# Kernel tuning notes

Measured on AMD Instinct MI355X. Metric: run time of the kernel, lower is better.

Reference implementation:

```python
import jax, jax.numpy as jnp
import numpy as np

LN_EPS = 1e-5
ATT_EPS = 1e-6

def layer_norm(x, scale, bias):
    mu = jnp.mean(x, axis=-1, keepdims=True)
    var = jnp.mean(jnp.square(x - mu), axis=-1, keepdims=True)
    return (x - mu) * jax.lax.rsqrt(var + LN_EPS) * scale + bias

def setup_inputs() -> dict:
    key = jax.random.key(0)
    ks = jax.random.split(key, 8)
    N, C, H = 16384, 1024, 8
    s = 0.02
    return {
        "x": jax.random.normal(ks[0], (N, C), dtype=jnp.float32),
        "Wq": jax.random.normal(ks[1], (C, C), dtype=jnp.float32) * s,
        "Wkv": jax.random.normal(ks[2], (C, 2 * C), dtype=jnp.float32) * s,
        "ln1_scale": jnp.ones((C,), dtype=jnp.float32),
        "ln1_bias": jnp.zeros((C,), dtype=jnp.float32),
        "W1": jax.random.normal(ks[3], (C, C), dtype=jnp.float32) * s,
        "b1": jnp.zeros((C,), dtype=jnp.float32),
        "W2": jax.random.normal(ks[4], (C, C), dtype=jnp.float32) * s,
        "b2": jnp.zeros((C,), dtype=jnp.float32),
        "ln2_scale": jnp.ones((C,), dtype=jnp.float32),
        "ln2_bias": jnp.zeros((C,), dtype=jnp.float32),
    }

def reference(x, Wq, Wkv, ln1_scale, ln1_bias, W1, b1, W2, b2, ln2_scale, ln2_bias):
    H = 8
    N, C = x.shape
    d = C // H
    # QKV projections; torch .view(-1, d, heads) splits last dim as (d, H)
    q = (x @ Wq).reshape(N, d, H)
    kv = x @ Wkv  # [N, 2C]
    k = kv[:, :C].reshape(N, d, H)
    v = kv[:, C:].reshape(N, d, H)
    # Kernelized linear attention per head (phi = elu + 1), global segment (bi=None)
    phi_q = jax.nn.elu(q) + 1.0
    phi_k = jax.nn.elu(k) + 1.0
    kv_sum = jnp.einsum('ndh,neh->deh', phi_k, v)      # [d, d, H]
    z = jnp.sum(phi_k, axis=0)                          # [d, H]
    num = jnp.einsum('ndh,deh->neh', phi_q, kv_sum)     # [N, d, H]
    den = jnp.einsum('ndh,dh->nh', phi_q, z)            # [N, H]
    t = (num / (den[:, None, :] + ATT_EPS)).reshape(N, C)
    # AddNorm (beta=False, dropout=0): ln(t + x)
    y = layer_norm(t + x, ln1_scale, ln1_bias)
    # FFN: Linear -> GELU (exact) -> Linear
    h = jax.nn.gelu(y @ W1 + b1, approximate=False)
    f = h @ W2 + b2
    return layer_norm(f + y, ln2_scale, ln2_bias)
```

## Files before the change

kernel.cpp:

```cpp
#include <hip/hip_runtime.h>
#include <hip/hip_bf16.h>
#include <cstdint>
#include <cstddef>

typedef __bf16 bf16_t;
typedef bf16_t bf16x4 __attribute__((ext_vector_type(4)));
typedef bf16_t bf16x8 __attribute__((ext_vector_type(8)));
typedef float f32x4 __attribute__((ext_vector_type(4)));

static constexpr int NROWS = 16384;
static constexpr int CDIM  = 1024;

__device__ __forceinline__ int p6(int k) {
  return (k & 32) | ((k & 12) << 1) | ((k & 16) >> 2) | (k & 3);
}
__device__ __forceinline__ int p6i(int s) {
  return (s & 32) | ((s & 4) << 2) | ((s & 24) >> 1) | (s & 3);
}
__device__ __forceinline__ int permc(int c) {
  return (c & ~63) | p6(c & 63);
}


__device__ __forceinline__ void gload16(const bf16_t* g, bf16_t* l) {
  __builtin_amdgcn_global_load_lds((const __attribute__((address_space(1))) void*)g,
                                   (__attribute__((address_space(3))) void*)l, 16, 0, 0);
}

__device__ __forceinline__ bf16x8 ldsf128(const bf16_t* lds, int row, int ldbytes, int kbyte) {
  const char* p = (const char*)lds + row * ldbytes + (kbyte ^ ((row & 7) << 4));
  return *(const bf16x8*)p;
}

__device__ __forceinline__ float phi_fn(float v) {
  return v > 0.f ? v + 1.f : expf(v);
}
__device__ __forceinline__ float gelu_fn(float v) {
  return 0.5f * v * (1.f + erff(v * 0.70710678118654752f));
}


__global__ void cast_x_kernel(const float* __restrict__ x, bf16_t* __restrict__ xb, long nchunks) {
  long i = (long)blockIdx.x * blockDim.x + threadIdx.x;
  long stride = (long)gridDim.x * blockDim.x;
  for (long c = i; c < nchunks; c += stride) {
    long row = c >> 7;
    int p0 = (int)(c & 127) << 3;
    int group = p0 & ~63;
    int ccl = (p0 >> 3) & 7;
    int klo = ((ccl & 4) << 3) | ((ccl & 3) << 2);
    const float* src = x + row * 1024 + group + klo;
    float4 a = *(const float4*)src;
    float4 b = *(const float4*)(src + 16);
    bf16x8 o;
    o[0] = (bf16_t)a.x; o[1] = (bf16_t)a.y; o[2] = (bf16_t)a.z; o[3] = (bf16_t)a.w;
    o[4] = (bf16_t)b.x; o[5] = (bf16_t)b.y; o[6] = (bf16_t)b.z; o[7] = (bf16_t)b.w;
    *(bf16x8*)(xb + row * 1024 + p0) = o;
  }
}

__global__ void prep_w_kernel(const float* __restrict__ Wq, const float* __restrict__ Wkv,
                              const float* __restrict__ W1, const float* __restrict__ W2,
                              bf16_t* __restrict__ wqkv_bt, bf16_t* __restrict__ w1bt,
                              bf16_t* __restrict__ w2bt) {
  __shared__ float tile[64][65];
  int mode = blockIdx.z;
  const float* src; int ld; bf16_t* dst; int permute;
  if (mode == 0)      { src = Wq;          ld = 1024; dst = wqkv_bt;                       permute = 1; }
  else if (mode == 1) { src = Wkv;         ld = 2048; dst = wqkv_bt + (size_t)1024 * 1024; permute = 1; }
  else if (mode == 2) { src = Wkv + 1024;  ld = 2048; dst = wqkv_bt + (size_t)2048 * 1024; permute = 1; }
  else if (mode == 3) { src = W1;          ld = 1024; dst = w1bt;                          permute = 0; }
  else                { src = W2;          ld = 1024; dst = w2bt;                          permute = 0; }
  int r0 = blockIdx.x * 64, c0 = blockIdx.y * 64;
  int tid = threadIdx.x;
#pragma unroll
  for (int i = 0; i < 16; i++) {
    int idx = i * 256 + tid; int rr = idx >> 6, cc = idx & 63;
    tile[rr][cc] = src[(size_t)(r0 + rr) * ld + c0 + cc];
  }
  __syncthreads();
#pragma unroll
  for (int i = 0; i < 16; i++) {
    int idx = i * 256 + tid; int cc = idx >> 6, rr = idx & 63;
    int c = c0 + cc;
    int a = permute ? (((c & 7) << 7) | (c >> 3)) : c;
    dst[(size_t)a * 1024 + r0 + p6(rr)] = (bf16_t)tile[rr][cc];
  }
}


template<int MODE>
__global__ __launch_bounds__(256, 4)
void gemm_bt_kernel(const bf16_t* __restrict__ A, const bf16_t* __restrict__ Bt,
                    const float* __restrict__ bias,
                    bf16_t* __restrict__ o0, bf16_t* __restrict__ o1, bf16_t* __restrict__ o2,
                    int M, int N, int K)
{
  __shared__ bf16_t As[128 * 64];
  __shared__ bf16_t Bs[128 * 64];
  const int tid  = threadIdx.x;
  const int lane = tid & 63;
  const int wave = tid >> 6;
  const int wr = (wave >> 1) * 64, wc = (wave & 1) * 64;
  const int l15 = lane & 15, g = lane >> 4;
  const int row0 = blockIdx.x * 128, col0 = blockIdx.y * 128;
  const int cb = wave * 256;
  f32x4 acc[4][4] = {};

  for (int kt = 0; kt < K; kt += 64) {
    __syncthreads();
#pragma unroll
    for (int it = 0; it < 4; ++it) {
      int ch = cb + it * 64 + lane;
      int r = ch >> 3;
      int csrc = (ch & 7) ^ (r & 7);
      gload16(A  + (size_t)(row0 + r) * K + kt + csrc * 8, As + (size_t)(cb + it * 64) * 8);
      gload16(Bt + (size_t)(col0 + r) * K + kt + csrc * 8, Bs + (size_t)(cb + it * 64) * 8);
    }
    __syncthreads();
#pragma unroll
    for (int ks = 0; ks < 2; ++ks) {
      bf16x8 af[4], bfr[4];
#pragma unroll
      for (int i = 0; i < 4; i++) af[i]  = ldsf128(As, wr + i * 16 + l15, 128, ks * 64 + 16 * g);
#pragma unroll
      for (int i = 0; i < 4; i++) bfr[i] = ldsf128(Bs, wc + i * 16 + l15, 128, ks * 64 + 16 * g);
#pragma unroll
      for (int i = 0; i < 4; i++)
#pragma unroll
        for (int j = 0; j < 4; j++)
          acc[i][j] = __builtin_amdgcn_mfma_f32_16x16x32_bf16(af[i], bfr[j], acc[i][j], 0, 0, 0);
    }
  }

#pragma unroll
  for (int i = 0; i < 4; i++) {
    int rbase = row0 + wr + i * 16 + g * 4;
#pragma unroll
    for (int j = 0; j < 4; j++) {
      int col = col0 + wc + j * 16 + l15;
      f32x4 v = acc[i][j];
      if constexpr (MODE == 0) {
        int seg = col >> 10;
        int cl  = permc(col & 1023);
        bf16_t* dst = (seg == 0) ? o0 : (seg == 1 ? o1 : o2);
#pragma unroll
        for (int rr = 0; rr < 4; rr++) {
          float val = v[rr];
          if (seg != 2) val = phi_fn(val);
          dst[(size_t)(rbase + rr) * 1024 + cl] = (bf16_t)val;
        }
      } else if constexpr (MODE == 1) {
        float bv = bias[col];
        int cs = permc(col);
#pragma unroll
        for (int rr = 0; rr < 4; rr++)
          o0[(size_t)(rbase + rr) * 1024 + cs] = (bf16_t)gelu_fn(v[rr] + bv);
      } else {
        float bv = bias[col];
#pragma unroll
        for (int rr = 0; rr < 4; rr++)
          o0[(size_t)(rbase + rr) * 1024 + col] = (bf16_t)(v[rr] + bv);
      }
    }
  }
}


__global__ __launch_bounds__(256, 4)
void kvsum_kernel(const bf16_t* __restrict__ phik, const bf16_t* __restrict__ vb,
                  float* __restrict__ P, float* __restrict__ Zp)
{
  __shared__ bf16_t kls[64 * 128];
  __shared__ bf16_t vls[64 * 128];
  const int h = blockIdx.y;
  const int c = blockIdx.x;
  const int n0 = c * 256;
  const int tid = threadIdx.x;
  const int lane = tid & 63, wave = tid >> 6;
  const int cb = wave * 256;
  const int ek0 = (tid >> 4) * 8, ev0 = (tid & 15) * 8;
  float acc[8][8] = {};
  float zacc[8] = {};

  for (int nt = 0; nt < 4; ++nt) {
    __syncthreads();
#pragma unroll
    for (int it = 0; it < 4; ++it) {
      int ch = cb + it * 64 + lane;
      int r = ch >> 4, c16 = ch & 15;
      const size_t gsrc = (size_t)(n0 + nt * 64 + r) * 1024 + h * 128 + c16 * 8;
      gload16(phik + gsrc, kls + (size_t)(cb + it * 64) * 8);
      gload16(vb   + gsrc, vls + (size_t)(cb + it * 64) * 8);
    }
    __syncthreads();
#pragma unroll 2
    for (int n = 0; n < 64; n++) {
      bf16x8 a8 = *(const bf16x8*)(kls + n * 128 + ek0);
      bf16x8 b8 = *(const bf16x8*)(vls + n * 128 + ev0);
      float a[8], b[8];
#pragma unroll
      for (int i = 0; i < 8; i++) { a[i] = (float)a8[i]; b[i] = (float)b8[i]; }
      if ((tid & 15) == 0) {
#pragma unroll
        for (int i = 0; i < 8; i++) zacc[i] += a[i];
      }
#pragma unroll
      for (int i = 0; i < 8; i++)
#pragma unroll
        for (int j = 0; j < 8; j++) acc[i][j] += a[i] * b[j];
    }
  }
  float* pb = P + ((size_t)h * 64 + c) * 16384;
#pragma unroll
  for (int i = 0; i < 8; i++) {
    *(float4*)(pb + (ek0 + i) * 128 + ev0)     = *(float4*)&acc[i][0];
    *(float4*)(pb + (ek0 + i) * 128 + ev0 + 4) = *(float4*)&acc[i][4];
  }
  if ((tid & 15) == 0) {
    float* zb = Zp + ((size_t)h * 64 + c) * 128;
#pragma unroll
    for (int i = 0; i < 8; i++) zb[ek0 + i] = zacc[i];
  }
}

__global__ void reduce_kvsum_kernel(const float* __restrict__ P, const float* __restrict__ Zp,
                                    bf16_t* __restrict__ Mbt, float* __restrict__ z)
{
  int i = blockIdx.x * 256 + threadIdx.x;
  int h = i >> 14, ds = (i >> 7) & 127, fs = i & 127;
  const float* p = P + (size_t)h * 64 * 16384 + (size_t)ds * 128 + fs;
  float s = 0.f;
#pragma unroll 8
  for (int c = 0; c < 64; ++c) s += p[(size_t)c * 16384];
  int fl = (fs & 64) | p6i(fs & 63);
  Mbt[(size_t)h * 16384 + fl * 128 + ds] = (bf16_t)s;
  if (i < 1024) {
    int hh = i >> 7, dd = i & 127;
    const float* q = Zp + (size_t)hh * 64 * 128 + dd;
    float sz = 0.f;
#pragma unroll 8
    for (int c = 0; c < 64; ++c) sz += q[c * 128];
    z[i] = sz;
  }
}


__global__ __launch_bounds__(256, 2)
void attn_t_kernel(const bf16_t* __restrict__ phiq, const bf16_t* __restrict__ Mbt,
                   const float* __restrict__ z, bf16_t* __restrict__ tout)
{
  __shared__ bf16_t As[64 * 128];
  __shared__ bf16_t Bs[128 * 128];
  __shared__ float  zs[128];
  __shared__ float  dens[64];
  int h = blockIdx.y, row0 = blockIdx.x * 64;
  int tid = threadIdx.x, lane = tid & 63, wave = tid >> 6;
  int wr = (wave >> 1) * 32, wc = (wave & 1) * 64;
  int l15 = lane & 15, g = lane >> 4;

#pragma unroll
  for (int it = 0; it < 4; ++it) {
    int ch = it * 256 + tid;
    int r = ch >> 4, c8 = ch & 15;
    int cs = c8 ^ (r & 7);
    *(bf16x8*)(As + r * 128 + cs * 8) = *(const bf16x8*)(phiq + (size_t)(row0 + r) * 1024 + h * 128 + c8 * 8);
  }
#pragma unroll
  for (int it = 0; it < 8; ++it) {
    int ch = it * 256 + tid;
    int r = ch >> 4, c8 = ch & 15;
    int cs = c8 ^ (r & 7);
    *(bf16x8*)(Bs + r * 128 + cs * 8) = *(const bf16x8*)(Mbt + (size_t)h * 16384 + ch * 8);
  }
  if (tid < 128) zs[tid] = z[h * 128 + tid];
  __syncthreads();

  f32x4 acc[2][4] = {};
#pragma unroll
  for (int ks = 0; ks < 4; ++ks) {
    bf16x8 af[2], bfr[4];
#pragma unroll
    for (int i = 0; i < 2; i++) af[i]  = ldsf128(As, wr + i * 16 + l15, 256, ks * 64 + 16 * g);
#pragma unroll
    for (int j = 0; j < 4; j++) bfr[j] = ldsf128(Bs, wc + j * 16 + l15, 256, ks * 64 + 16 * g);
#pragma unroll
    for (int i = 0; i < 2; i++)
#pragma unroll
      for (int j = 0; j < 4; j++)
        acc[i][j] = __builtin_amdgcn_mfma_f32_16x16x32_bf16(af[i], bfr[j], acc[i][j], 0, 0, 0);
  }

  if (tid < 64) {
    float s = 0.f;
    const char* p = (const char*)As + tid * 256;
    int sw = (tid & 7) << 4;
    for (int d0 = 0; d0 < 128; ++d0) {
      int d = (d0 + tid) & 127;
      bf16_t kv = *(const bf16_t*)(p + ((2 * d) ^ sw));
      s += (float)kv * zs[d];
    }
    dens[tid] = s;
  }
  __syncthreads();

#pragma unroll
  for (int i = 0; i < 2; i++) {
    int lr = wr + i * 16 + g * 4;
#pragma unroll
    for (int j = 0; j < 4; j++) {
      int col = h * 128 + wc + j * 16 + l15;
      f32x4 v = acc[i][j];
#pragma unroll
      for (int rr = 0; rr < 4; rr++) {
        float den = dens[lr + rr] + 1e-6f;
        tout[(size_t)(row0 + lr + rr) * 1024 + col] = (bf16_t)(v[rr] / den);
      }
    }
  }
}


__global__ __launch_bounds__(256, 2)
void ln1_kernel(const bf16_t* __restrict__ t, const float* __restrict__ x,
                const float* __restrict__ gma, const float* __restrict__ bta,
                bf16_t* __restrict__ y)
{
  __shared__ float s[1024];
  __shared__ float rsum[4], rsq[4];
  int n = blockIdx.x, tid = threadIdx.x;
#pragma unroll
  for (int k = 0; k < 4; k++) {
    int p = k * 256 + tid;
    float tv = (float)t[(size_t)n * 1024 + p];
    int c = ((p & 127) << 3) | (p >> 7);
    s[c] = tv;
  }
  __syncthreads();
  float sum = 0.f, sq = 0.f, sv[4];
#pragma unroll
  for (int k = 0; k < 4; k++) {
    int c = k * 256 + tid;
    float v = s[c] + x[(size_t)n * 1024 + c];
    sv[k] = v; sum += v; sq += v * v;
  }
#pragma unroll
  for (int o = 32; o > 0; o >>= 1) { sum += __shfl_down(sum, o); sq += __shfl_down(sq, o); }
  if ((tid & 63) == 0) { rsum[tid >> 6] = sum; rsq[tid >> 6] = sq; }
  __syncthreads();
  sum = rsum[0] + rsum[1] + rsum[2] + rsum[3];
  sq  = rsq[0] + rsq[1] + rsq[2] + rsq[3];
  float mu = sum * (1.f / 1024.f);
  float var = sq * (1.f / 1024.f) - mu * mu;
  float rs = rsqrtf(var + 1e-5f);
#pragma unroll
  for (int k = 0; k < 4; k++) {
    int c = k * 256 + tid;
    y[(size_t)n * 1024 + permc(c)] = (bf16_t)((sv[k] - mu) * rs * gma[c] + bta[c]);
  }
}

__global__ __launch_bounds__(256, 2)
void ln2_kernel(const bf16_t* __restrict__ f, const bf16_t* __restrict__ y,
                const float* __restrict__ gma, const float* __restrict__ bta,
                float* __restrict__ out)
{
  __shared__ float rsum[4], rsq[4];
  int n = blockIdx.x, tid = threadIdx.x;
  float sum = 0.f, sq = 0.f, sv[4];
#pragma unroll
  for (int k = 0; k < 4; k++) {
    int c = k * 256 + tid;
    float v = (float)f[(size_t)n * 1024 + c] + (float)y[(size_t)n * 1024 + permc(c)];
    sv[k] = v; sum += v; sq += v * v;
  }
#pragma unroll
  for (int o = 32; o > 0; o >>= 1) { sum += __shfl_down(sum, o); sq += __shfl_down(sq, o); }
  if ((tid & 63) == 0) { rsum[tid >> 6] = sum; rsq[tid >> 6] = sq; }
  __syncthreads();
  sum = rsum[0] + rsum[1] + rsum[2] + rsum[3];
  sq  = rsq[0] + rsq[1] + rsq[2] + rsq[3];
  float mu = sum * (1.f / 1024.f);
  float var = sq * (1.f / 1024.f) - mu * mu;
  float rs = rsqrtf(var + 1e-5f);
#pragma unroll
  for (int k = 0; k < 4; k++) {
    int c = k * 256 + tid;
    out[(size_t)n * 1024 + c] = (sv[k] - mu) * rs * gma[c] + bta[c];
  }
}


extern "C" void kernel_launch(void* const* d_in, const int* in_sizes, int n_in,
                              void* d_out, int out_size, void* d_ws, size_t ws_size,
                              hipStream_t stream)
{
  const float* x    = (const float*)d_in[0];
  const float* Wq   = (const float*)d_in[1];
  const float* Wkv  = (const float*)d_in[2];
  const float* g1   = (const float*)d_in[3];
  const float* bt1  = (const float*)d_in[4];
  const float* W1   = (const float*)d_in[5];
  const float* b1   = (const float*)d_in[6];
  const float* W2   = (const float*)d_in[7];
  const float* b2   = (const float*)d_in[8];
  const float* g2   = (const float*)d_in[9];
  const float* bt2  = (const float*)d_in[10];
  float* out = (float*)d_out;

  char* ws = (char*)d_ws;
  size_t off = 0;
  auto alloc = [&](size_t bytes) { void* p = ws + off; off += (bytes + 255) & ~(size_t)255; return p; };

  const size_t NC2 = (size_t)NROWS * CDIM * 2;
  bf16_t* xb    = (bf16_t*)alloc(NC2);
  bf16_t* wqkv  = (bf16_t*)alloc((size_t)3072 * 1024 * 2);
  bf16_t* w1bt  = (bf16_t*)alloc((size_t)1024 * 1024 * 2);
  bf16_t* w2bt  = (bf16_t*)alloc((size_t)1024 * 1024 * 2);
  bf16_t* phiq  = (bf16_t*)alloc(NC2);
  bf16_t* phik  = (bf16_t*)alloc(NC2);
  bf16_t* vbuf  = (bf16_t*)alloc(NC2);
  bf16_t* ybuf  = (bf16_t*)alloc(NC2);
  float*  Zp    = (float*)alloc(262144 + 4096);
  float*  zbuf  = Zp + 65536;
  bf16_t* Mbt   = (bf16_t*)alloc(262144);
  float*  Pbuf  = (float*)xb;
  bf16_t* tbuf  = xb;
  bf16_t* hbuf  = phik;
  bf16_t* fbuf  = vbuf;

  cast_x_kernel<<<2048, 256, 0, stream>>>(x, xb, (long)NROWS * CDIM / 8);
  prep_w_kernel<<<dim3(16, 16, 5), 256, 0, stream>>>(Wq, Wkv, W1, W2, wqkv, w1bt, w2bt);

  gemm_bt_kernel<0><<<dim3(128, 24), 256, 0, stream>>>(xb, wqkv, nullptr, phiq, phik, vbuf,
                                                       NROWS, 3072, 1024);
  kvsum_kernel<<<dim3(64, 8), 256, 0, stream>>>(phik, vbuf, Pbuf, Zp);
  reduce_kvsum_kernel<<<512, 256, 0, stream>>>(Pbuf, Zp, Mbt, zbuf);
  attn_t_kernel<<<dim3(256, 8), 256, 0, stream>>>(phiq, Mbt, zbuf, tbuf);
  ln1_kernel<<<NROWS, 256, 0, stream>>>(tbuf, x, g1, bt1, ybuf);

  gemm_bt_kernel<1><<<dim3(128, 8), 256, 0, stream>>>(ybuf, w1bt, b1, hbuf, nullptr, nullptr,
                                                      NROWS, 1024, 1024);
  gemm_bt_kernel<2><<<dim3(128, 8), 256, 0, stream>>>(hbuf, w2bt, b2, fbuf, nullptr, nullptr,
                                                      NROWS, 1024, 1024);
  ln2_kernel<<<NROWS, 256, 0, stream>>>(fbuf, ybuf, g2, bt2, out);
}
```

Baseline: 360.5 us.

## Replace 128x128 GEMM with 256x256 triple-buffered MFMA kernel

Replaces the three GEMMs with a 256x256-tile, 512-thread kernel. It triple-buffers K-slices of 32 in LDS using direct global-to-LDS loads, uses one barrier per step with explicit vmcnt waits, and raises wave priority around the MFMA block. Block indices are swizzled for L2 locality. The bigger tiles cut global traffic per FLOP and overlap loads with compute, at the cost of more registers and LDS, fewer blocks (256 for the FFN GEMMs), and hardcoded K=1024. The attention kernel's occupancy hint is also raised to 3.

```diff
diff --git a/kernel.cpp b/kernel.cpp
--- a/kernel.cpp
+++ b/kernel.cpp
@@ -25,11 +25,6 @@
 __device__ __forceinline__ void gload16(const bf16_t* g, bf16_t* l) {
   __builtin_amdgcn_global_load_lds((const __attribute__((address_space(1))) void*)g,
                                    (__attribute__((address_space(3))) void*)l, 16, 0, 0);
-}
-
-__device__ __forceinline__ bf16x8 ldsf128(const bf16_t* lds, int row, int ldbytes, int kbyte) {
-  const char* p = (const char*)lds + row * ldbytes + (kbyte ^ ((row & 7) << 4));
-  return *(const bf16x8*)p;
 }
 
 __device__ __forceinline__ float phi_fn(float v) {
@@ -90,55 +85,78 @@
 
 
 template<int MODE>
-__global__ __launch_bounds__(256, 4)
-void gemm_bt_kernel(const bf16_t* __restrict__ A, const bf16_t* __restrict__ Bt,
+__global__ __launch_bounds__(512, 2)
+void gemm256_kernel(const bf16_t* __restrict__ A, const bf16_t* __restrict__ Bt,
                     const float* __restrict__ bias,
                     bf16_t* __restrict__ o0, bf16_t* __restrict__ o1, bf16_t* __restrict__ o2,
-                    int M, int N, int K)
-{
-  __shared__ bf16_t As[128 * 64];
-  __shared__ bf16_t Bs[128 * 64];
-  const int tid  = threadIdx.x;
-  const int lane = tid & 63;
-  const int wave = tid >> 6;
-  const int wr = (wave >> 1) * 64, wc = (wave & 1) * 64;
+                    int tn_count)
+{
+  __shared__ bf16_t lds[3 * 16384];
+  const int tid = threadIdx.x, lane = tid & 63, wave = tid >> 6;
   const int l15 = lane & 15, g = lane >> 4;
-  const int row0 = blockIdx.x * 128, col0 = blockIdx.y * 128;
-  const int cb = wave * 256;
-  f32x4 acc[4][4] = {};
-
-  for (int kt = 0; kt < K; kt += 64) {
-    __syncthreads();
-#pragma unroll
-    for (int it = 0; it < 4; ++it) {
-      int ch = cb + it * 64 + lane;
-      int r = ch >> 3;
-      int csrc = (ch & 7) ^ (r & 7);
-      gload16(A  + (size_t)(row0 + r) * K + kt + csrc * 8, As + (size_t)(cb + it * 64) * 8);
-      gload16(Bt + (size_t)(col0 + r) * K + kt + csrc * 8, Bs + (size_t)(cb + it * 64) * 8);
-    }
-    __syncthreads();
-#pragma unroll
-    for (int ks = 0; ks < 2; ++ks) {
-      bf16x8 af[4], bfr[4];
-#pragma unroll
-      for (int i = 0; i < 4; i++) af[i]  = ldsf128(As, wr + i * 16 + l15, 128, ks * 64 + 16 * g);
-#pragma unroll
-      for (int i = 0; i < 4; i++) bfr[i] = ldsf128(Bs, wc + i * 16 + l15, 128, ks * 64 + 16 * g);
-#pragma unroll
-      for (int i = 0; i < 4; i++)
-#pragma unroll
-        for (int j = 0; j < 4; j++)
-          acc[i][j] = __builtin_amdgcn_mfma_f32_16x16x32_bf16(af[i], bfr[j], acc[i][j], 0, 0, 0);
-    }
-  }
-
-#pragma unroll
-  for (int i = 0; i < 4; i++) {
-    int rbase = row0 + wr + i * 16 + g * 4;
+  const int cpx = gridDim.x >> 3;
+  int swz = (blockIdx.x & 7) * cpx + (blockIdx.x >> 3);
+  const int row0 = (swz / tn_count) * 256, col0 = (swz % tn_count) * 256;
+  const int wrb = (wave >> 2) * 8, wcb = (wave & 3) * 4;
+  f32x4 acc[8][4] = {};
+
+  const size_t aoff0 = (size_t)(row0 + wave * 16 + l15) * 1024 + g * 8;
+  const size_t aoff1 = aoff0 + (size_t)128 * 1024;
+  const size_t boff0 = (size_t)(col0 + wave * 16 + l15) * 1024 + g * 8;
+  const size_t boff1 = boff0 + (size_t)128 * 1024;
+  const int wd0 = wave * 512, wd1 = (8 + wave) * 512;
+
+  auto stage = [&](int t, bf16_t* buf) {
+    const int kts = t * 32;
+    gload16(A  + aoff0 + kts, buf + wd0);
+    gload16(A  + aoff1 + kts, buf + wd1);
+    gload16(Bt + boff0 + kts, buf + 8192 + wd0);
+    gload16(Bt + boff1 + kts, buf + 8192 + wd1);
+  };
+
+  stage(0, lds);
+  stage(1, lds + 16384);
+  asm volatile("s_waitcnt vmcnt(4)" ::: "memory");
+  __builtin_amdgcn_sched_barrier(0);
+  __builtin_amdgcn_s_barrier();
+  __builtin_amdgcn_sched_barrier(0);
+
+  int cur = 0, nxt = 1, stg = 2;
+  for (int t = 0; t < 32; ++t) {
+    if (t < 30) {
+      stage(t + 2, lds + stg * 16384);
+      __builtin_amdgcn_sched_barrier(0);
+    }
+    const bf16_t* bA = lds + cur * 16384;
+    const bf16_t* bB = bA + 8192;
+    bf16x8 af[8], bfr[4];
+#pragma unroll
+    for (int i = 0; i < 8; i++) af[i]  = *(const bf16x8*)(bA + (wrb + i) * 512 + lane * 8);
+#pragma unroll
+    for (int j = 0; j < 4; j++) bfr[j] = *(const bf16x8*)(bB + (wcb + j) * 512 + lane * 8);
+    __builtin_amdgcn_s_setprio(1);
+#pragma unroll
+    for (int i = 0; i < 8; i++)
+#pragma unroll
+      for (int j = 0; j < 4; j++)
+        acc[i][j] = __builtin_amdgcn_mfma_f32_16x16x32_bf16(af[i], bfr[j], acc[i][j], 0, 0, 0);
+    __builtin_amdgcn_s_setprio(0);
+    if (t < 30)       asm volatile("s_waitcnt vmcnt(4)" ::: "memory");
+    else if (t == 30) asm volatile("s_waitcnt vmcnt(0)" ::: "memory");
+    __builtin_amdgcn_sched_barrier(0);
+    if (t < 31) {
+      __builtin_amdgcn_s_barrier();
+      __builtin_amdgcn_sched_barrier(0);
+    }
+    int tmp = cur; cur = nxt; nxt = stg; stg = tmp;
+  }
+
+#pragma unroll
+  for (int i = 0; i < 8; i++) {
+    int rbase = row0 + (wave >> 2) * 128 + i * 16 + g * 4;
 #pragma unroll
     for (int j = 0; j < 4; j++) {
-      int col = col0 + wc + j * 16 + l15;
+      int col = col0 + (wave & 3) * 64 + j * 16 + l15;
       f32x4 v = acc[i][j];
       if constexpr (MODE == 0) {
         int seg = col >> 10;
@@ -246,7 +264,12 @@
 }
 
 
-__global__ __launch_bounds__(256, 2)
+__device__ __forceinline__ bf16x8 ldsf128(const bf16_t* lds, int row, int ldbytes, int kbyte) {
+  const char* p = (const char*)lds + row * ldbytes + (kbyte ^ ((row & 7) << 4));
+  return *(const bf16x8*)p;
+}
+
+__global__ __launch_bounds__(256, 3)
 void attn_t_kernel(const bf16_t* __restrict__ phiq, const bf16_t* __restrict__ Mbt,
                    const float* __restrict__ z, bf16_t* __restrict__ tout)
 {
@@ -432,16 +455,13 @@
   cast_x_kernel<<<2048, 256, 0, stream>>>(x, xb, (long)NROWS * CDIM / 8);
   prep_w_kernel<<<dim3(16, 16, 5), 256, 0, stream>>>(Wq, Wkv, W1, W2, wqkv, w1bt, w2bt);
 
-  gemm_bt_kernel<0><<<dim3(128, 24), 256, 0, stream>>>(xb, wqkv, nullptr, phiq, phik, vbuf,
-                                                       NROWS, 3072, 1024);
+  gemm256_kernel<0><<<64 * 12, 512, 0, stream>>>(xb, wqkv, nullptr, phiq, phik, vbuf, 12);
   kvsum_kernel<<<dim3(64, 8), 256, 0, stream>>>(phik, vbuf, Pbuf, Zp);
   reduce_kvsum_kernel<<<512, 256, 0, stream>>>(Pbuf, Zp, Mbt, zbuf);
   attn_t_kernel<<<dim3(256, 8), 256, 0, stream>>>(phiq, Mbt, zbuf, tbuf);
   ln1_kernel<<<NROWS, 256, 0, stream>>>(tbuf, x, g1, bt1, ybuf);
 
-  gemm_bt_kernel<1><<<dim3(128, 8), 256, 0, stream>>>(ybuf, w1bt, b1, hbuf, nullptr, nullptr,
-                                                      NROWS, 1024, 1024);
-  gemm_bt_kernel<2><<<dim3(128, 8), 256, 0, stream>>>(hbuf, w2bt, b2, fbuf, nullptr, nullptr,
-                                                      NROWS, 1024, 1024);
+  gemm256_kernel<1><<<64 * 4, 512, 0, stream>>>(ybuf, w1bt, b1, hbuf, nullptr, nullptr, 4);
+  gemm256_kernel<2><<<64 * 4, 512, 0, stream>>>(hbuf, w2bt, b2, fbuf, nullptr, nullptr, 4);
   ln2_kernel<<<NROWS, 256, 0, stream>>>(fbuf, ybuf, g2, bt2, out);
 }
```

Measured after the change: 400.4 us. 11.1% more time.
